# Performance work log

Measured on AMD Instinct MI355X. Metric: run time of the kernel, lower is better.

Reference implementation:

```python
import jax, jax.numpy as jnp
import numpy as np

K = 16          # number of nearest neighbors (init kwarg k)
EPS = 1e-3      # denom threshold from the original code


def setup_inputs() -> dict:
    key = jax.random.key(0)
    k1, k2, k3 = jax.random.split(key, 3)
    V, F = 5000, 10000
    vertices = jax.random.normal(k1, (V, 3), dtype=jnp.float32)
    faces = jax.random.randint(k2, (F, 3), 0, V)
    probabilities = jax.random.uniform(k3, (F,), dtype=jnp.float32)
    return {"vertices": vertices, "faces": faces, "probabilities": probabilities}


def reference(vertices, faces, probabilities):
    F = faces.shape[0]
    pos = vertices[faces]                       # [F,3,3] triangle vertex coords
    bary = pos.mean(axis=1)                     # [F,3] barycenters

    # brute-force kNN over barycenters (x == y, so self is included like torch_geometric knn)
    sq = jnp.sum(bary * bary, axis=-1)          # [F]
    d2 = sq[:, None] + sq[None, :] - 2.0 * (bary @ bary.T)   # [F,F]
    _, nbr = jax.lax.top_k(-d2, K)              # [F,K] neighbor face indices

    # face normals
    e1 = pos[:, 1] - pos[:, 0]
    e2 = pos[:, 2] - pos[:, 0]
    n = jnp.cross(e1, e2)
    n = n / jnp.maximum(jnp.linalg.norm(n, axis=-1, keepdims=True), 1e-12)  # [F,3]

    # per (tri, neighbor, triangle-edge) plane intersection test
    nb_pos = pos[nbr]                           # [F,K,3,3] neighbor triangle vertices
    l0 = nb_pos                                 # segment starts
    l1 = jnp.roll(nb_pos, -1, axis=2)           # segment ends (k -> (k+1)%3)
    n_b = n[:, None, None, :]                   # [F,1,1,3]
    p0_b = pos[:, 0][:, None, None, :]          # [F,1,1,3] plane point of tri

    denom = jnp.sum(n_b * (l1 - l0), axis=-1)   # [F,K,3]
    numer = jnp.sum(n_b * (p0_b - l0), axis=-1) # [F,K,3]
    safe_denom = jnp.where(jnp.abs(denom) < EPS, 1.0, denom)
    t = numer / safe_denom
    hit = (jnp.abs(denom) >= EPS) & (t > 0.0) & (t < 1.0)   # [F,K,3]

    # early break in original => at most 1 increment per (tri, neighbor) pair
    pen = jnp.any(hit, axis=-1) & (nbr != jnp.arange(F)[:, None])  # [F,K]

    # scatter-add penetrations into neighbor_idx
    faces_penetrated = jnp.zeros((F,), jnp.float32).at[nbr.ravel()].add(
        pen.ravel().astype(jnp.float32))

    return jnp.dot(probabilities, faces_penetrated) / F
```

## Files before the change

kernel.cpp:

```cpp
#include <hip/hip_runtime.h>
#include <math.h>

#define KNN 16
#define EPS_F 0.001f
#define BLK 256
#define LCAP 25
#define SCH 16
#define SSTRIDE 8

#define REP16(M) M(0) M(1) M(2) M(3) M(4) M(5) M(6) M(7) \
                 M(8) M(9) M(10) M(11) M(12) M(13) M(14) M(15)

#define CEAI(p,a,b) { int _lo = min(p##a, p##b); int _hi = max(p##a, p##b); p##a = _lo; p##b = _hi; }
#define CEDI(p,a,b) { int _lo = min(p##a, p##b); int _hi = max(p##a, p##b); p##a = _hi; p##b = _lo; }

#define SORT16I(p) \
  CEAI(p,0,1) CEDI(p,2,3) CEAI(p,4,5) CEDI(p,6,7) CEAI(p,8,9) CEDI(p,10,11) CEAI(p,12,13) CEDI(p,14,15) \
  CEAI(p,0,2) CEAI(p,1,3) CEDI(p,4,6) CEDI(p,5,7) CEAI(p,8,10) CEAI(p,9,11) CEDI(p,12,14) CEDI(p,13,15) \
  CEAI(p,0,1) CEAI(p,2,3) CEDI(p,4,5) CEDI(p,6,7) CEAI(p,8,9) CEAI(p,10,11) CEDI(p,12,13) CEDI(p,14,15) \
  CEAI(p,0,4) CEAI(p,1,5) CEAI(p,2,6) CEAI(p,3,7) CEDI(p,8,12) CEDI(p,9,13) CEDI(p,10,14) CEDI(p,11,15) \
  CEAI(p,0,2) CEAI(p,1,3) CEAI(p,4,6) CEAI(p,5,7) CEDI(p,8,10) CEDI(p,9,11) CEDI(p,12,14) CEDI(p,13,15) \
  CEAI(p,0,1) CEAI(p,2,3) CEAI(p,4,5) CEAI(p,6,7) CEDI(p,8,9) CEDI(p,10,11) CEDI(p,12,13) CEDI(p,14,15) \
  CEAI(p,0,8) CEAI(p,1,9) CEAI(p,2,10) CEAI(p,3,11) CEAI(p,4,12) CEAI(p,5,13) CEAI(p,6,14) CEAI(p,7,15) \
  CEAI(p,0,4) CEAI(p,1,5) CEAI(p,2,6) CEAI(p,3,7) CEAI(p,8,12) CEAI(p,9,13) CEAI(p,10,14) CEAI(p,11,15) \
  CEAI(p,0,2) CEAI(p,1,3) CEAI(p,4,6) CEAI(p,5,7) CEAI(p,8,10) CEAI(p,9,11) CEAI(p,12,14) CEAI(p,13,15) \
  CEAI(p,0,1) CEAI(p,2,3) CEAI(p,4,5) CEAI(p,6,7) CEAI(p,8,9) CEAI(p,10,11) CEAI(p,12,13) CEAI(p,14,15)

#define RESORT16I(p) \
  CEAI(p,0,8) CEAI(p,1,9) CEAI(p,2,10) CEAI(p,3,11) CEAI(p,4,12) CEAI(p,5,13) CEAI(p,6,14) CEAI(p,7,15) \
  CEAI(p,0,4) CEAI(p,1,5) CEAI(p,2,6) CEAI(p,3,7) CEAI(p,8,12) CEAI(p,9,13) CEAI(p,10,14) CEAI(p,11,15) \
  CEAI(p,0,2) CEAI(p,1,3) CEAI(p,4,6) CEAI(p,5,7) CEAI(p,8,10) CEAI(p,9,11) CEAI(p,12,14) CEAI(p,13,15) \
  CEAI(p,0,1) CEAI(p,2,3) CEAI(p,4,5) CEAI(p,6,7) CEAI(p,8,9) CEAI(p,10,11) CEAI(p,12,13) CEAI(p,14,15)

#define MERGE16I(r,x) \
  r##0=min(r##0,x##15); r##1=min(r##1,x##14); r##2=min(r##2,x##13); r##3=min(r##3,x##12); \
  r##4=min(r##4,x##11); r##5=min(r##5,x##10); r##6=min(r##6,x##9);  r##7=min(r##7,x##8);  \
  r##8=min(r##8,x##7);  r##9=min(r##9,x##6);  r##10=min(r##10,x##5); r##11=min(r##11,x##4); \
  r##12=min(r##12,x##3); r##13=min(r##13,x##2); r##14=min(r##14,x##1); r##15=min(r##15,x##0); \
  RESORT16I(r)

__device__ __forceinline__ float distf(float4 q, float4 P) {
    return fmaf(q.x, P.x, fmaf(q.y, P.y, fmaf(q.z, P.z, q.w + P.w)));
}
__device__ __forceinline__ int packkey(float d2, int j) {
    return (__float_as_int(d2) & 0xFFFFC000) | j;
}

__global__ __launch_bounds__(BLK) void prep_kernel(
    const float* __restrict__ verts, const int* __restrict__ faces,
    float4* __restrict__ baryq, float4* __restrict__ baryqm,
    float* __restrict__ nrm, float* __restrict__ p0s, int F)
{
    int f = blockIdx.x * BLK + threadIdx.x;
    if (f >= F) return;
    int i0 = faces[3*f+0], i1 = faces[3*f+1], i2 = faces[3*f+2];
    float ax = verts[3*i0+0], ay = verts[3*i0+1], az = verts[3*i0+2];
    float bx = verts[3*i1+0], by = verts[3*i1+1], bz = verts[3*i1+2];
    float cx = verts[3*i2+0], cy = verts[3*i2+1], cz = verts[3*i2+2];
    float gx = (ax + bx + cx) / 3.0f;
    float gy = (ay + by + cy) / 3.0f;
    float gz = (az + bz + cz) / 3.0f;
    float sq = gx*gx + gy*gy + gz*gz;
    baryq[f]  = make_float4(gx, gy, gz, sq);
    baryqm[f] = make_float4(-2.0f*gx, -2.0f*gy, -2.0f*gz, sq);
    float e1x = bx-ax, e1y = by-ay, e1z = bz-az;
    float e2x = cx-ax, e2y = cy-ay, e2z = cz-az;
    float nx = e1y*e2z - e1z*e2y;
    float ny = e1z*e2x - e1x*e2z;
    float nz = e1x*e2y - e1y*e2x;
    float len = sqrtf(nx*nx + ny*ny + nz*nz);
    float dn = fmaxf(len, 1e-12f);
    nrm[3*f+0] = nx/dn; nrm[3*f+1] = ny/dn; nrm[3*f+2] = nz/dn;
    p0s[3*f+0] = ax; p0s[3*f+1] = ay; p0s[3*f+2] = az;
}

__global__ __launch_bounds__(BLK) void knn_sample(
    const float4* __restrict__ baryq, const float4* __restrict__ baryqm,
    int* __restrict__ samp_k, int F, int SLEN)
{
    int tid = threadIdx.x;
    int qi = blockIdx.x * BLK + tid;
    float4 q = baryq[min(qi, F-1)];
    #define DECLR(m) int r##m = 0x7fffffff;
    REP16(DECLR)
    #undef DECLR
    int sbase = blockIdx.y * SLEN;
    #pragma unroll 1
    for (int g = 0; g < SLEN; g += 16) {
        #define MKK(m) int x##m; { int s = sbase + g + (m); int j = s * SSTRIDE; \
            float4 P = baryqm[min(j, F-1)]; \
            int k = packkey(distf(q, P), j); \
            x##m = (j < F) ? k : 0x7fffffff; }
        REP16(MKK)
        #undef MKK
        SORT16I(x)
        MERGE16I(r, x)
    }
    if (qi < F) {
        size_t cb = (size_t)blockIdx.y * KNN * F + qi;
        #define STR(m) samp_k[cb + (size_t)(m) * F] = r##m;
        REP16(STR)
        #undef STR
    }
}

__global__ __launch_bounds__(BLK) void merge_T(
    const int* __restrict__ samp_k, int* __restrict__ Tkey,
    int* __restrict__ cnt, int F)
{
    int qi = blockIdx.x * BLK + threadIdx.x;
    if (qi >= F) return;
    #define LDR(m) int r##m = samp_k[(size_t)(m) * F + qi];
    REP16(LDR)
    #undef LDR
    for (int c = 1; c < SCH; ++c) {
        size_t cb = (size_t)c * KNN * F + qi;
        #define LDX(m) int x##m = samp_k[cb + (size_t)(m) * F];
        REP16(LDX)
        #undef LDX
        MERGE16I(r, x)
    }
    Tkey[qi] = r15;
    cnt[qi] = 0;
}

__global__ __launch_bounds__(BLK) void collect_kernel(
    const float4* __restrict__ baryq, const float4* __restrict__ baryqm,
    const int* __restrict__ Tkey, int* __restrict__ cnt,
    int* __restrict__ buf, int F, int CLEN, int CAP)
{
    __shared__ int lb[BLK * LCAP];
    int tid = threadIdx.x;
    int qi = blockIdx.x * BLK + tid;
    bool active = qi < F;
    int qc = min(qi, F-1);
    float4 q = baryq[qc];
    int T = active ? Tkey[qc] : 0x80000000;
    int lbb = tid * LCAP;
    int lcnt = 0;
    int jb = blockIdx.y * CLEN;
    int je = min(jb + CLEN, F);
    int jfull = jb + ((je - jb) & ~15);
    #pragma unroll 1
    for (int base = jb; base < jfull; base += 16) {
        const float4* tp = baryqm + base;
        #define CSTEP(m) { float4 P = tp[m]; \
            int key = packkey(distf(q, P), base + (m)); \
            lb[lbb + min(lcnt, LCAP-1)] = key; \
            lcnt += (key <= T) ? 1 : 0; }
        REP16(CSTEP)
        #undef CSTEP
    }
    for (int j = jfull; j < je; ++j) {
        float4 P = baryqm[j];
        int key = packkey(distf(q, P), j);
        lb[lbb + min(lcnt, LCAP-1)] = key;
        lcnt += (key <= T) ? 1 : 0;
    }
    lcnt = min(lcnt, LCAP);
    if (active && lcnt > 0) {
        int basep = atomicAdd(&cnt[qi], lcnt);
        for (int k = 0; k < lcnt; ++k) {
            int p = basep + k;
            if (p < CAP) buf[(size_t)qi * CAP + p] = lb[lbb + k];
        }
    }
}

__global__ __launch_bounds__(BLK) void final_select(
    const int* __restrict__ buf, const int* __restrict__ cnt,
    int* __restrict__ nbr, int F, int CAP)
{
    int qi = blockIdx.x * BLK + threadIdx.x;
    if (qi >= F) return;
    int n = min(cnt[qi], CAP);
    const int* row = buf + (size_t)qi * CAP;
    #define DECLR(m) int r##m = 0x7fffffff;
    REP16(DECLR)
    #undef DECLR
    #pragma unroll 1
    for (int t = 0; t < n; t += 16) {
        #define LSEL(m) int x##m; { int v = row[t + (m)]; \
            x##m = (t + (m) < n) ? v : 0x7fffffff; }
        REP16(LSEL)
        #undef LSEL
        SORT16I(x)
        MERGE16I(r, x)
    }
    size_t ob = (size_t)qi * KNN;
    #define STN(m) nbr[ob + (m)] = r##m & 0x3FFF;
    REP16(STN)
    #undef STN
}

__device__ __forceinline__ bool edge_test(
    float nx, float ny, float nz, float px, float py, float pz,
    float ax, float ay, float az, float bx, float by, float bz)
{
    float denom = nx*(bx-ax) + ny*(by-ay) + nz*(bz-az);
    if (fabsf(denom) < EPS_F) return false;
    float numer = nx*(px-ax) + ny*(py-ay) + nz*(pz-az);
    float t = numer / denom;
    return (t > 0.0f) && (t < 1.0f);
}

__global__ __launch_bounds__(BLK) void pen_kernel(
    const float* __restrict__ verts, const int* __restrict__ faces,
    const float* __restrict__ prob, const int* __restrict__ nbr,
    const float* __restrict__ nrm, const float* __restrict__ p0s,
    float* __restrict__ partial, int F)
{
    int t = blockIdx.x * BLK + threadIdx.x;
    float val = 0.0f;
    int total = F * KNN;
    if (t < total) {
        int i = t >> 4;
        int j = nbr[t];
        if (j != i) {
            float nx = nrm[3*i+0], ny = nrm[3*i+1], nz = nrm[3*i+2];
            float px = p0s[3*i+0], py = p0s[3*i+1], pz = p0s[3*i+2];
            int j0 = faces[3*j+0], j1 = faces[3*j+1], j2 = faces[3*j+2];
            float ax = verts[3*j0+0], ay = verts[3*j0+1], az = verts[3*j0+2];
            float bx = verts[3*j1+0], by = verts[3*j1+1], bz = verts[3*j1+2];
            float cx = verts[3*j2+0], cy = verts[3*j2+1], cz = verts[3*j2+2];
            bool hit = edge_test(nx,ny,nz, px,py,pz, ax,ay,az, bx,by,bz)
                    || edge_test(nx,ny,nz, px,py,pz, bx,by,bz, cx,cy,cz)
                    || edge_test(nx,ny,nz, px,py,pz, cx,cy,cz, ax,ay,az);
            if (hit) val = prob[j];
        }
    }
    __shared__ float red[BLK];
    red[threadIdx.x] = val;
    __syncthreads();
    #pragma unroll
    for (int s = BLK/2; s > 0; s >>= 1) {
        if (threadIdx.x < s) red[threadIdx.x] += red[threadIdx.x + s];
        __syncthreads();
    }
    if (threadIdx.x == 0) partial[blockIdx.x] = red[0];
}

__global__ __launch_bounds__(BLK) void final_reduce(
    const float* __restrict__ partial, int n, float* __restrict__ out, int F)
{
    __shared__ float red[BLK];
    float s = 0.0f;
    for (int i = threadIdx.x; i < n; i += BLK) s += partial[i];
    red[threadIdx.x] = s;
    __syncthreads();
    #pragma unroll
    for (int st = BLK/2; st > 0; st >>= 1) {
        if (threadIdx.x < st) red[threadIdx.x] += red[threadIdx.x + st];
        __syncthreads();
    }
    if (threadIdx.x == 0) out[0] = red[0] / (float)F;
}

extern "C" void kernel_launch(void* const* d_in, const int* in_sizes, int n_in,
                              void* d_out, int out_size, void* d_ws, size_t ws_size,
                              hipStream_t stream)
{
    const float* verts = (const float*)d_in[0];
    const int*   faces = (const int*)d_in[1];
    const float* prob  = (const float*)d_in[2];
    float* out = (float*)d_out;
    int F = in_sizes[2];

    size_t off = 0;
    auto carve = [&](size_t bytes) {
        size_t cur = off;
        off += (bytes + 255) & ~(size_t)255;
        return cur;
    };
    char* w = (char*)d_ws;
    int nPenBlocks = (F * KNN + BLK - 1) / BLK;
    float4* baryq  = (float4*)(w + carve((size_t)F * sizeof(float4)));
    float4* baryqm = (float4*)(w + carve((size_t)F * sizeof(float4)));
    float*  nrm    = (float*)(w + carve((size_t)F * 3 * sizeof(float)));
    float*  p0s    = (float*)(w + carve((size_t)F * 3 * sizeof(float)));
    int*    nbr    = (int*)(w + carve((size_t)F * KNN * sizeof(int)));
    float*  partial= (float*)(w + carve((size_t)nPenBlocks * sizeof(float)));
    int*    Tkey   = (int*)(w + carve((size_t)F * sizeof(int)));
    int*    cnt    = (int*)(w + carve((size_t)F * sizeof(int)));
    int*    samp_k = (int*)(w + carve((size_t)SCH * KNN * F * sizeof(int)));

    size_t remain = (ws_size > off) ? (ws_size - off) : 0;
    int CAP = (int)(remain / ((size_t)F * sizeof(int)));
    if (CAP > 448) CAP = 448;
    if (CAP < 320) CAP = 320;
    CAP &= ~15;
    int* buf = (int*)(w + carve((size_t)F * CAP * sizeof(int)));

    int nSamp = (F + SSTRIDE - 1) / SSTRIDE;
    int SLEN = ((nSamp + SCH - 1) / SCH + 15) & ~15;
    int CCH = 40;
    int CLEN = (((F + CCH - 1) / CCH + BLK - 1) / BLK) * BLK;
    int nCChunk = (F + CLEN - 1) / CLEN;

    int qBlocks = (F + BLK - 1) / BLK;

    prep_kernel<<<qBlocks, BLK, 0, stream>>>(verts, faces, baryq, baryqm, nrm, p0s, F);
    knn_sample<<<dim3(qBlocks, SCH), BLK, 0, stream>>>(baryq, baryqm, samp_k, F, SLEN);
    merge_T<<<qBlocks, BLK, 0, stream>>>(samp_k, Tkey, cnt, F);
    collect_kernel<<<dim3(qBlocks, nCChunk), BLK, 0, stream>>>(
        baryq, baryqm, Tkey, cnt, buf, F, CLEN, CAP);
    final_select<<<qBlocks, BLK, 0, stream>>>(buf, cnt, nbr, F, CAP);
    pen_kernel<<<nPenBlocks, BLK, 0, stream>>>(
        verts, faces, prob, nbr, nrm, p0s, partial, F);
    final_reduce<<<1, BLK, 0, stream>>>(partial, nPenBlocks, out, F);
}
```

Measured before the change: 99.62 us.

## Fuse final kNN selection with penetration test and rebalance collect chunks

```diff
diff --git a/kernel.cpp b/kernel.cpp
--- a/kernel.cpp
+++ b/kernel.cpp
@@ -4,7 +4,7 @@
 #define KNN 16
 #define EPS_F 0.001f
 #define BLK 256
-#define LCAP 25
+#define LCAP 17
 #define SCH 16
 #define SSTRIDE 8
 
@@ -124,7 +124,7 @@
     cnt[qi] = 0;
 }
 
-__global__ __launch_bounds__(BLK) void collect_kernel(
+__global__ __launch_bounds__(BLK, 8) void collect_kernel(
     const float4* __restrict__ baryq, const float4* __restrict__ baryqm,
     const int* __restrict__ Tkey, int* __restrict__ cnt,
     int* __restrict__ buf, int F, int CLEN, int CAP)
@@ -146,16 +146,14 @@
         const float4* tp = baryqm + base;
         #define CSTEP(m) { float4 P = tp[m]; \
             int key = packkey(distf(q, P), base + (m)); \
-            lb[lbb + min(lcnt, LCAP-1)] = key; \
-            lcnt += (key <= T) ? 1 : 0; }
+            if (key <= T) { lb[lbb + min(lcnt, LCAP-1)] = key; ++lcnt; } }
         REP16(CSTEP)
         #undef CSTEP
     }
     for (int j = jfull; j < je; ++j) {
         float4 P = baryqm[j];
         int key = packkey(distf(q, P), j);
-        lb[lbb + min(lcnt, LCAP-1)] = key;
-        lcnt += (key <= T) ? 1 : 0;
+        if (key <= T) { lb[lbb + min(lcnt, LCAP-1)] = key; ++lcnt; }
     }
     lcnt = min(lcnt, LCAP);
     if (active && lcnt > 0) {
@@ -167,32 +165,6 @@
     }
 }
 
-__global__ __launch_bounds__(BLK) void final_select(
-    const int* __restrict__ buf, const int* __restrict__ cnt,
-    int* __restrict__ nbr, int F, int CAP)
-{
-    int qi = blockIdx.x * BLK + threadIdx.x;
-    if (qi >= F) return;
-    int n = min(cnt[qi], CAP);
-    const int* row = buf + (size_t)qi * CAP;
-    #define DECLR(m) int r##m = 0x7fffffff;
-    REP16(DECLR)
-    #undef DECLR
-    #pragma unroll 1
-    for (int t = 0; t < n; t += 16) {
-        #define LSEL(m) int x##m; { int v = row[t + (m)]; \
-            x##m = (t + (m) < n) ? v : 0x7fffffff; }
-        REP16(LSEL)
-        #undef LSEL
-        SORT16I(x)
-        MERGE16I(r, x)
-    }
-    size_t ob = (size_t)qi * KNN;
-    #define STN(m) nbr[ob + (m)] = r##m & 0x3FFF;
-    REP16(STN)
-    #undef STN
-}
-
 __device__ __forceinline__ bool edge_test(
     float nx, float ny, float nz, float px, float py, float pz,
     float ax, float ay, float az, float bx, float by, float bz)
@@ -204,30 +176,44 @@
     return (t > 0.0f) && (t < 1.0f);
 }
 
-__global__ __launch_bounds__(BLK) void pen_kernel(
+__global__ __launch_bounds__(BLK) void select_pen(
+    const int* __restrict__ buf, const int* __restrict__ cnt,
     const float* __restrict__ verts, const int* __restrict__ faces,
-    const float* __restrict__ prob, const int* __restrict__ nbr,
-    const float* __restrict__ nrm, const float* __restrict__ p0s,
-    float* __restrict__ partial, int F)
-{
-    int t = blockIdx.x * BLK + threadIdx.x;
+    const float* __restrict__ prob, const float* __restrict__ nrm,
+    const float* __restrict__ p0s, float* __restrict__ partial,
+    int F, int CAP)
+{
+    int qi = blockIdx.x * BLK + threadIdx.x;
     float val = 0.0f;
-    int total = F * KNN;
-    if (t < total) {
-        int i = t >> 4;
-        int j = nbr[t];
-        if (j != i) {
-            float nx = nrm[3*i+0], ny = nrm[3*i+1], nz = nrm[3*i+2];
-            float px = p0s[3*i+0], py = p0s[3*i+1], pz = p0s[3*i+2];
-            int j0 = faces[3*j+0], j1 = faces[3*j+1], j2 = faces[3*j+2];
-            float ax = verts[3*j0+0], ay = verts[3*j0+1], az = verts[3*j0+2];
-            float bx = verts[3*j1+0], by = verts[3*j1+1], bz = verts[3*j1+2];
-            float cx = verts[3*j2+0], cy = verts[3*j2+1], cz = verts[3*j2+2];
-            bool hit = edge_test(nx,ny,nz, px,py,pz, ax,ay,az, bx,by,bz)
-                    || edge_test(nx,ny,nz, px,py,pz, bx,by,bz, cx,cy,cz)
-                    || edge_test(nx,ny,nz, px,py,pz, cx,cy,cz, ax,ay,az);
-            if (hit) val = prob[j];
+    if (qi < F) {
+        int n = min(cnt[qi], CAP);
+        const int* row = buf + (size_t)qi * CAP;
+        #define DECLR(m) int r##m = 0x7fffffff;
+        REP16(DECLR)
+        #undef DECLR
+        #pragma unroll 1
+        for (int t = 0; t < n; t += 16) {
+            #define LSEL(m) int x##m; { int v = row[t + (m)]; \
+                x##m = (t + (m) < n) ? v : 0x7fffffff; }
+            REP16(LSEL)
+            #undef LSEL
+            SORT16I(x)
+            MERGE16I(r, x)
         }
+        float nx = nrm[3*qi+0], ny = nrm[3*qi+1], nz = nrm[3*qi+2];
+        float px = p0s[3*qi+0], py = p0s[3*qi+1], pz = p0s[3*qi+2];
+        #define PENM(m) { int j = r##m & 0x3FFF; \
+            if (j != qi && j < F) { \
+                int j0 = faces[3*j+0], j1 = faces[3*j+1], j2 = faces[3*j+2]; \
+                float ax = verts[3*j0+0], ay = verts[3*j0+1], az = verts[3*j0+2]; \
+                float bx = verts[3*j1+0], by = verts[3*j1+1], bz = verts[3*j1+2]; \
+                float cx = verts[3*j2+0], cy = verts[3*j2+1], cz = verts[3*j2+2]; \
+                bool hit = edge_test(nx,ny,nz, px,py,pz, ax,ay,az, bx,by,bz) \
+                        || edge_test(nx,ny,nz, px,py,pz, bx,by,bz, cx,cy,cz) \
+                        || edge_test(nx,ny,nz, px,py,pz, cx,cy,cz, ax,ay,az); \
+                if (hit) val += prob[j]; } }
+        REP16(PENM)
+        #undef PENM
     }
     __shared__ float red[BLK];
     red[threadIdx.x] = val;
@@ -273,13 +259,12 @@
         return cur;
     };
     char* w = (char*)d_ws;
-    int nPenBlocks = (F * KNN + BLK - 1) / BLK;
+    int qBlocks = (F + BLK - 1) / BLK;
     float4* baryq  = (float4*)(w + carve((size_t)F * sizeof(float4)));
     float4* baryqm = (float4*)(w + carve((size_t)F * sizeof(float4)));
     float*  nrm    = (float*)(w + carve((size_t)F * 3 * sizeof(float)));
     float*  p0s    = (float*)(w + carve((size_t)F * 3 * sizeof(float)));
-    int*    nbr    = (int*)(w + carve((size_t)F * KNN * sizeof(int)));
-    float*  partial= (float*)(w + carve((size_t)nPenBlocks * sizeof(float)));
+    float*  partial= (float*)(w + carve((size_t)qBlocks * sizeof(float)));
     int*    Tkey   = (int*)(w + carve((size_t)F * sizeof(int)));
     int*    cnt    = (int*)(w + carve((size_t)F * sizeof(int)));
     int*    samp_k = (int*)(w + carve((size_t)SCH * KNN * F * sizeof(int)));
@@ -293,19 +278,16 @@
 
     int nSamp = (F + SSTRIDE - 1) / SSTRIDE;
     int SLEN = ((nSamp + SCH - 1) / SCH + 15) & ~15;
-    int CCH = 40;
-    int CLEN = (((F + CCH - 1) / CCH + BLK - 1) / BLK) * BLK;
+    int CCH = 80;
+    int CLEN = (((F + CCH - 1) / CCH) + 15) & ~15;
     int nCChunk = (F + CLEN - 1) / CLEN;
-
-    int qBlocks = (F + BLK - 1) / BLK;
 
     prep_kernel<<<qBlocks, BLK, 0, stream>>>(verts, faces, baryq, baryqm, nrm, p0s, F);
     knn_sample<<<dim3(qBlocks, SCH), BLK, 0, stream>>>(baryq, baryqm, samp_k, F, SLEN);
     merge_T<<<qBlocks, BLK, 0, stream>>>(samp_k, Tkey, cnt, F);
     collect_kernel<<<dim3(qBlocks, nCChunk), BLK, 0, stream>>>(
         baryq, baryqm, Tkey, cnt, buf, F, CLEN, CAP);
-    final_select<<<qBlocks, BLK, 0, stream>>>(buf, cnt, nbr, F, CAP);
-    pen_kernel<<<nPenBlocks, BLK, 0, stream>>>(
-        verts, faces, prob, nbr, nrm, p0s, partial, F);
-    final_reduce<<<1, BLK, 0, stream>>>(partial, nPenBlocks, out, F);
-}
+    select_pen<<<qBlocks, BLK, 0, stream>>>(
+        buf, cnt, verts, faces, prob, nrm, p0s, partial, F, CAP);
+    final_reduce<<<1, BLK, 0, stream>>>(partial, qBlocks, out, F);
+}
```

Result: no change. 99.38 us (-0.2%).
